# Performance work log

Hardware: AMD Instinct MI355X
Metric: run time of the kernel (lower is better)

## Reference

```python
import jax, jax.numpy as jnp
import numpy as np

B = 2_097_152  # batch of (ttm, logm) option quotes
J = 5          # hidden width from hidden_sizes=[5,5,5]


def setup_inputs() -> dict:
    key = jax.random.key(0)
    ks = jax.random.split(key, 14)
    d = jnp.float32
    s = 0.01  # torch init: normal(mean=0, std=0.01)
    inp = {
        "ttm": jax.random.uniform(ks[0], (B, 1), d),
        "logm": jax.random.normal(ks[1], (B, 1), d),
        "weights_logm": jax.random.normal(ks[2], (1, J), d) * s,
        "bias_logm": jax.random.normal(ks[3], (1, J), d) * s,
        "weights_ttm": jax.random.normal(ks[4], (1, J), d) * s,
        "bias_ttm": jax.random.normal(ks[5], (1, J), d) * s,
        "weights_exp": jax.random.normal(ks[6], (J, 1), d) * s,
        "bias_exp": jax.random.normal(ks[7], (1, J), d) * s,
        # nn.Linear default init ~ U(-1/sqrt(J), 1/sqrt(J))
        "W1": jax.random.uniform(ks[8], (J, J), d, -1.0, 1.0) / np.sqrt(J),
        "b1": jax.random.uniform(ks[9], (J,), d, -1.0, 1.0) / np.sqrt(J),
        "W2": jax.random.uniform(ks[10], (J, J), d, -1.0, 1.0) / np.sqrt(J),
        "b2": jax.random.uniform(ks[11], (J,), d, -1.0, 1.0) / np.sqrt(J),
        "Wo": jax.random.uniform(ks[12], (1, J), d, -1.0, 1.0) / np.sqrt(J),
        "bo": jax.random.uniform(ks[13], (1,), d, -1.0, 1.0) / np.sqrt(J),
    }
    return inp


def _forward(ttm, logm, weights_logm, bias_logm, weights_ttm, bias_ttm,
             weights_exp, bias_exp, W1, b1, W2, b2, Wo, bo):
    # smile transform of log-moneyness: sqrt(x*tanh(x+0.5) + tanh(-x/2) + 5e-4)
    x = bias_logm + logm @ jnp.exp(weights_logm)                     # [B, J]
    term_logm = jnp.sqrt(x * jnp.tanh(x + 0.5) + jnp.tanh(-x / 2) + 0.0005)
    term_ttm = jax.nn.sigmoid(bias_ttm + ttm @ jnp.exp(weights_ttm))  # [B, J]
    h = (term_logm * term_ttm) @ jnp.exp(weights_exp) + bias_exp      # [B,1]+[1,J] -> [B, J]
    h = jax.nn.softplus(h @ W1.T + b1)
    h = jax.nn.softplus(h @ W2.T + b2)
    return h @ Wo.T + bo                                              # [B, 1]


def reference(ttm, logm, weights_logm, bias_logm, weights_ttm, bias_ttm,
              weights_exp, bias_exp, W1, b1, W2, b2, Wo, bo):
    params = (weights_logm, bias_logm, weights_ttm, bias_ttm,
              weights_exp, bias_exp, W1, b1, W2, b2, Wo, bo)

    def out_sum(t, l):
        return jnp.sum(_forward(t, l, *params))

    output = _forward(ttm, logm, *params)                 # [B, 1]
    # grad of sum(output) wrt ttm and logm (rows independent -> per-sample grads)
    grad_ttm1, grad_logm1 = jax.grad(out_sum, argnums=(0, 1))(ttm, logm)
    # second derivative wrt logm: grad of sum(grad_logm1)
    grad_logm2 = jax.grad(
        lambda l: jnp.sum(jax.grad(out_sum, argnums=1)(ttm, l))
    )(logm)
    return (output, grad_ttm1, grad_logm1, grad_logm2)
```

## Files before the change

kernel.cpp:

```cpp
#include <hip/hip_runtime.h>
#include <math.h>

#define J 5

#if defined(__HIP_DEVICE_COMPILE__) && __has_builtin(__builtin_amdgcn_rcpf)
__device__ __forceinline__ float fastrcp(float x) { return __builtin_amdgcn_rcpf(x); }
#else
__device__ __forceinline__ float fastrcp(float x) { return 1.0f / x; }
#endif

#if defined(__HIP_DEVICE_COMPILE__) && __has_builtin(__builtin_amdgcn_rsqf)
__device__ __forceinline__ float fastrsq(float x) { return __builtin_amdgcn_rsqf(x); }
#else
__device__ __forceinline__ float fastrsq(float x) { return 1.0f / sqrtf(x); }
#endif

__device__ __forceinline__ float fast_tanh_from_e2y(float e2y) {
    return fmaf(-2.0f, fastrcp(e2y + 1.0f), 1.0f);
}

__global__ __launch_bounds__(256) void smile_kernel(
    const float* __restrict__ ttm,     const float* __restrict__ logm,
    const float* __restrict__ w_logm,  const float* __restrict__ b_logm,
    const float* __restrict__ w_ttm,   const float* __restrict__ b_ttm,
    const float* __restrict__ w_exp,   const float* __restrict__ b_exp,
    const float* __restrict__ W1,      const float* __restrict__ b1,
    const float* __restrict__ W2,      const float* __restrict__ b2,
    const float* __restrict__ Wo,      const float* __restrict__ bo,
    float* __restrict__ out, int n)
{
    const int tid = blockIdx.x * blockDim.x + threadIdx.x;
    const int i0  = tid * 4;
    if (i0 >= n) return;

    float ewl[J], bl[J], ewt[J], bt[J], ewe[J], wte[J];
#pragma unroll
    for (int j = 0; j < J; ++j) {
        ewl[j] = __expf(w_logm[j]);
        bl[j]  = b_logm[j];
        ewt[j] = __expf(w_ttm[j]);
        bt[j]  = b_ttm[j];
        ewe[j] = __expf(w_exp[j]);
        wte[j] = ewt[j] * ewe[j];
    }
    float r1[J], c1[J];
#pragma unroll
    for (int i = 0; i < J; ++i) {
        float r = 0.0f, c = b1[i];
#pragma unroll
        for (int j = 0; j < J; ++j) {
            const float w = W1[i * J + j];
            r += w;
            c = fmaf(w, b_exp[j], c);
        }
        r1[i] = r; c1[i] = c;
    }
    const float bo0 = bo[0];

    const float4 T4 = ((const float4*)ttm)[tid];
    const float4 L4 = ((const float4*)logm)[tid];
    float Ts[4] = {T4.x, T4.y, T4.z, T4.w};
    float Ls[4] = {L4.x, L4.y, L4.z, L4.w};
    float O0[4], O1[4], O2[4], O3[4];

#pragma unroll
    for (int k = 0; k < 4; ++k) {
        const float L = Ls[k], T = Ts[k];

        float s = 0.0f, sL = 0.0f, sLL = 0.0f, sT = 0.0f;
#pragma unroll
        for (int j = 0; j < J; ++j) {
            const float x  = fmaf(L, ewl[j], bl[j]);
            const float t1 = fast_tanh_from_e2y(__expf(fmaf(2.0f, x, 1.0f)));
            const float t2 = fast_tanh_from_e2y(__expf(-x));
            const float m1 = fmaf(-t1, t1, 1.0f);
            const float m2 = fmaf(-t2, t2, 1.0f);
            const float u  = fmaf(x, t1, t2) + 5.0e-4f;
            const float xm1 = x * m1;
            const float ux  = fmaf(-0.5f, m2, t1 + xm1);
            const float uxx = fmaf(-0.5f * t2, m2, 2.0f * fmaf(-t1, xm1, m1));
            const float r   = fastrsq(u);
            const float tl  = u * r;
            const float i2  = 0.5f * r;
            const float ru  = r * r;
            const float tlL  = ux * ewl[j] * i2;
            const float tlLL = (ewl[j] * ewl[j]) * i2 * fmaf(-0.5f * ux, ux * ru, uxx);
            const float z   = fmaf(T, ewt[j], bt[j]);
            const float tt  = fastrcp(1.0f + __expf(-z));
            const float dtt = fmaf(-tt, tt, tt);
            const float A   = tt * ewe[j];
            s   = fmaf(tl,   A, s);
            sL  = fmaf(tlL,  A, sL);
            sLL = fmaf(tlLL, A, sLL);
            sT  = fmaf(tl * dtt, wte[j], sT);
        }

        float h1[J], h1L[J], h1LL[J], h1T[J];
#pragma unroll
        for (int i = 0; i < J; ++i) {
            const float a   = fmaf(s, r1[i], c1[i]);
            const float aL  = sL  * r1[i];
            const float aLL = sLL * r1[i];
            const float aT  = sT  * r1[i];
            const float sg  = fastrcp(1.0f + __expf(-a));
            const float sp  = a - __logf(sg);
            const float dsg = fmaf(-sg, sg, sg);
            h1[i]   = sp;
            h1L[i]  = sg * aL;
            h1LL[i] = fmaf(dsg * aL, aL, sg * aLL);
            h1T[i]  = sg * aT;
        }

        float o = bo0, oL = 0.0f, oLL = 0.0f, oT = 0.0f;
#pragma unroll
        for (int i = 0; i < J; ++i) {
            float g = b2[i], gL = 0.0f, gLL = 0.0f, gT = 0.0f;
#pragma unroll
            for (int j = 0; j < J; ++j) {
                const float w = W2[i * J + j];
                g   = fmaf(w, h1[j],   g);
                gL  = fmaf(w, h1L[j],  gL);
                gLL = fmaf(w, h1LL[j], gLL);
                gT  = fmaf(w, h1T[j],  gT);
            }
            const float sg  = fastrcp(1.0f + __expf(-g));
            const float sp  = g - __logf(sg);
            const float dsg = fmaf(-sg, sg, sg);
            const float wo  = Wo[i];
            o   = fmaf(wo, sp, o);
            oL  = fmaf(wo, sg * gL, oL);
            oLL = fmaf(wo, fmaf(dsg * gL, gL, sg * gLL), oLL);
            oT  = fmaf(wo, sg * gT, oT);
        }

        O0[k] = o;
        O1[k] = oT;
        O2[k] = oL;
        O3[k] = oLL;
    }

    ((float4*)(out))[tid]                       = make_float4(O0[0], O0[1], O0[2], O0[3]);
    ((float4*)(out + (size_t)n))[tid]           = make_float4(O1[0], O1[1], O1[2], O1[3]);
    ((float4*)(out + 2 * (size_t)n))[tid]       = make_float4(O2[0], O2[1], O2[2], O2[3]);
    ((float4*)(out + 3 * (size_t)n))[tid]       = make_float4(O3[0], O3[1], O3[2], O3[3]);
}

extern "C" void kernel_launch(void* const* d_in, const int* in_sizes, int n_in,
                              void* d_out, int out_size, void* d_ws, size_t ws_size,
                              hipStream_t stream) {
    const float* ttm    = (const float*)d_in[0];
    const float* logm   = (const float*)d_in[1];
    const float* w_logm = (const float*)d_in[2];
    const float* b_logm = (const float*)d_in[3];
    const float* w_ttm  = (const float*)d_in[4];
    const float* b_ttm  = (const float*)d_in[5];
    const float* w_exp  = (const float*)d_in[6];
    const float* b_exp  = (const float*)d_in[7];
    const float* W1     = (const float*)d_in[8];
    const float* b1     = (const float*)d_in[9];
    const float* W2     = (const float*)d_in[10];
    const float* b2     = (const float*)d_in[11];
    const float* Wo     = (const float*)d_in[12];
    const float* bo     = (const float*)d_in[13];
    float* out = (float*)d_out;

    const int n = in_sizes[0];
    const int threads = (n + 3) / 4;
    const int blocks  = (threads + 255) / 256;
    smile_kernel<<<blocks, 256, 0, stream>>>(
        ttm, logm, w_logm, b_logm, w_ttm, b_ttm, w_exp, b_exp,
        W1, b1, W2, b2, Wo, bo, out, n);
}
```

Before: 125.0 us.

## Precompute weight constants in setup kernel and factor derivative propagation algebraically

A tiny setup kernel now precomputes the exponentiated weights, folded layer-1 coefficients and squared terms into workspace, so the main kernel stops recomputing them in every thread. The derivative chain is restructured: because every layer-1 pre-activation depends on one scalar, first and second derivatives are factored into shared terms (q, p, Bq, Bp), which removes the separate L/LL/T accumulators. Both tanh terms are computed from a single exp of x, and softplus uses a numerically stable abs-based form. This trades an extra kernel launch and a clamp on x for fewer transcendentals and FMAs per sample.

```diff
diff --git a/kernel.cpp b/kernel.cpp
--- a/kernel.cpp
+++ b/kernel.cpp
@@ -15,134 +15,173 @@
 __device__ __forceinline__ float fastrsq(float x) { return 1.0f / sqrtf(x); }
 #endif
 
-__device__ __forceinline__ float fast_tanh_from_e2y(float e2y) {
-    return fmaf(-2.0f, fastrcp(e2y + 1.0f), 1.0f);
-}
-
-__global__ __launch_bounds__(256) void smile_kernel(
-    const float* __restrict__ ttm,     const float* __restrict__ logm,
-    const float* __restrict__ w_logm,  const float* __restrict__ b_logm,
-    const float* __restrict__ w_ttm,   const float* __restrict__ b_ttm,
-    const float* __restrict__ w_exp,   const float* __restrict__ b_exp,
-    const float* __restrict__ W1,      const float* __restrict__ b1,
-    const float* __restrict__ W2,      const float* __restrict__ b2,
-    const float* __restrict__ Wo,      const float* __restrict__ bo,
-    float* __restrict__ out, int n)
+__global__ void setup_kernel(const float* __restrict__ w_logm, const float* __restrict__ b_logm,
+                             const float* __restrict__ w_ttm,  const float* __restrict__ b_ttm,
+                             const float* __restrict__ w_exp,  const float* __restrict__ b_exp,
+                             const float* __restrict__ W1,     const float* __restrict__ b1,
+                             const float* __restrict__ W2,     const float* __restrict__ b2,
+                             const float* __restrict__ Wo,     const float* __restrict__ bo,
+                             float* __restrict__ c)
+{
+    const int j = threadIdx.x;
+    if (j >= J) return;
+    const float ewl = __expf(w_logm[j]);
+    const float ewt = __expf(w_ttm[j]);
+    const float ewe = __expf(w_exp[j]);
+    c[0  + j] = ewl;
+    c[5  + j] = b_logm[j];
+    c[10 + j] = ewl * ewl;
+    c[15 + j] = -ewt;
+    c[20 + j] = -b_ttm[j];
+    c[25 + j] = ewe;
+    c[30 + j] = ewt * ewe;
+    float r = 0.0f, cc = b1[j];
+#pragma unroll
+    for (int t = 0; t < J; ++t) {
+        const float w = W1[j * J + t];
+        r += w;
+        cc = fmaf(w, b_exp[t], cc);
+    }
+    c[35 + j] = r;
+    c[40 + j] = cc;
+    c[45 + j] = r * r;
+#pragma unroll
+    for (int t = 0; t < J; ++t) c[50 + j * J + t] = W2[j * J + t];
+    c[75 + j] = b2[j];
+    c[80 + j] = Wo[j];
+    if (j == 0) c[85] = bo[0];
+}
+
+__device__ __forceinline__ void softplus_sig(float a, float& sp, float& sg) {
+    const float aa = fabsf(a);
+    const float em = __expf(-aa);
+    const float w  = fastrcp(1.0f + em);
+    sp = fmaxf(a, 0.0f) + __logf(1.0f + em);
+    sg = (a >= 0.0f) ? w : 1.0f - w;
+}
+
+__global__ __launch_bounds__(256) void smile_main(
+    const float* __restrict__ ttm, const float* __restrict__ logm,
+    const float* __restrict__ c, float* __restrict__ out, int n)
 {
     const int tid = blockIdx.x * blockDim.x + threadIdx.x;
-    const int i0  = tid * 4;
-    if (i0 >= n) return;
-
-    float ewl[J], bl[J], ewt[J], bt[J], ewe[J], wte[J];
+    if (tid * 4 >= n) return;
+
+    float ewl[J], bl[J], ewl2[J], newt[J], nbt[J], ewe[J], wte[J];
 #pragma unroll
     for (int j = 0; j < J; ++j) {
-        ewl[j] = __expf(w_logm[j]);
-        bl[j]  = b_logm[j];
-        ewt[j] = __expf(w_ttm[j]);
-        bt[j]  = b_ttm[j];
-        ewe[j] = __expf(w_exp[j]);
-        wte[j] = ewt[j] * ewe[j];
-    }
-    float r1[J], c1[J];
-#pragma unroll
-    for (int i = 0; i < J; ++i) {
-        float r = 0.0f, c = b1[i];
-#pragma unroll
-        for (int j = 0; j < J; ++j) {
-            const float w = W1[i * J + j];
-            r += w;
-            c = fmaf(w, b_exp[j], c);
-        }
-        r1[i] = r; c1[i] = c;
-    }
-    const float bo0 = bo[0];
+        ewl[j]  = c[0  + j];
+        bl[j]   = c[5  + j];
+        ewl2[j] = c[10 + j];
+        newt[j] = c[15 + j];
+        nbt[j]  = c[20 + j];
+        ewe[j]  = c[25 + j];
+        wte[j]  = c[30 + j];
+    }
 
     const float4 T4 = ((const float4*)ttm)[tid];
     const float4 L4 = ((const float4*)logm)[tid];
-    float Ts[4] = {T4.x, T4.y, T4.z, T4.w};
-    float Ls[4] = {L4.x, L4.y, L4.z, L4.w};
-    float O0[4], O1[4], O2[4], O3[4];
-
+    const float Ts[4] = {T4.x, T4.y, T4.z, T4.w};
+    const float Ls[4] = {L4.x, L4.y, L4.z, L4.w};
+
+    float sA[4], sLA[4], sLLA[4], sTA[4];
 #pragma unroll
     for (int k = 0; k < 4; ++k) {
         const float L = Ls[k], T = Ts[k];
-
         float s = 0.0f, sL = 0.0f, sLL = 0.0f, sT = 0.0f;
 #pragma unroll
         for (int j = 0; j < J; ++j) {
-            const float x  = fmaf(L, ewl[j], bl[j]);
-            const float t1 = fast_tanh_from_e2y(__expf(fmaf(2.0f, x, 1.0f)));
-            const float t2 = fast_tanh_from_e2y(__expf(-x));
+            float x = fmaf(L, ewl[j], bl[j]);
+            x = fminf(fmaxf(x, -30.0f), 30.0f);
+            const float ex = __expf(x);
+            const float e2 = ex * ex;
+            const float t1 = fmaf(-2.0f, fastrcp(fmaf(2.7182818284590452f, e2, 1.0f)), 1.0f);
+            const float t2 = (1.0f - ex) * fastrcp(1.0f + ex);
             const float m1 = fmaf(-t1, t1, 1.0f);
             const float m2 = fmaf(-t2, t2, 1.0f);
-            const float u  = fmaf(x, t1, t2) + 5.0e-4f;
+            const float u  = fmaf(x, t1, t2 + 5.0e-4f);
             const float xm1 = x * m1;
             const float ux  = fmaf(-0.5f, m2, t1 + xm1);
             const float uxx = fmaf(-0.5f * t2, m2, 2.0f * fmaf(-t1, xm1, m1));
             const float r   = fastrsq(u);
             const float tl  = u * r;
             const float i2  = 0.5f * r;
-            const float ru  = r * r;
-            const float tlL  = ux * ewl[j] * i2;
-            const float tlLL = (ewl[j] * ewl[j]) * i2 * fmaf(-0.5f * ux, ux * ru, uxx);
-            const float z   = fmaf(T, ewt[j], bt[j]);
-            const float tt  = fastrcp(1.0f + __expf(-z));
+            const float h   = ux * (r * r);
+            const float zn  = fmaf(T, newt[j], nbt[j]);
+            const float tt  = fastrcp(1.0f + __expf(zn));
             const float dtt = fmaf(-tt, tt, tt);
-            const float A   = tt * ewe[j];
-            s   = fmaf(tl,   A, s);
-            sL  = fmaf(tlL,  A, sL);
-            sLL = fmaf(tlLL, A, sLL);
+            const float AA   = tt * ewe[j];
+            const float ewlA = ewl[j] * AA;
+            s   = fmaf(tl, AA, s);
+            sL  = fmaf(ux * i2, ewlA, sL);
+            const float inner = fmaf(-0.5f * ux, h, uxx);
+            sLL = fmaf(inner * i2, ewl[j] * ewlA, sLL);
             sT  = fmaf(tl * dtt, wte[j], sT);
+            (void)ewl2;
         }
-
-        float h1[J], h1L[J], h1LL[J], h1T[J];
+        sA[k] = s; sLA[k] = sL; sLLA[k] = sLL; sTA[k] = sT;
+    }
+
+    float r1[J], c1[J], r1sq[J], W2r[J * J], b2[J], wo[J];
+#pragma unroll
+    for (int j = 0; j < J; ++j) {
+        r1[j]   = c[35 + j];
+        c1[j]   = c[40 + j];
+        r1sq[j] = c[45 + j];
+        b2[j]   = c[75 + j];
+        wo[j]   = c[80 + j];
+    }
+#pragma unroll
+    for (int t = 0; t < J * J; ++t) W2r[t] = c[50 + t];
+    const float bo0 = c[85];
+
+    float O0[4], O1[4], O2[4], O3[4];
+#pragma unroll
+    for (int k = 0; k < 4; ++k) {
+        const float s = sA[k], sL = sLA[k], sLL = sLLA[k], sT = sTA[k];
+
+        float q[J], p[J], sp1[J];
 #pragma unroll
         for (int i = 0; i < J; ++i) {
-            const float a   = fmaf(s, r1[i], c1[i]);
-            const float aL  = sL  * r1[i];
-            const float aLL = sLL * r1[i];
-            const float aT  = sT  * r1[i];
-            const float sg  = fastrcp(1.0f + __expf(-a));
-            const float sp  = a - __logf(sg);
+            const float a = fmaf(s, r1[i], c1[i]);
+            float sp, sg;
+            softplus_sig(a, sp, sg);
+            sp1[i] = sp;
+            q[i]   = sg * r1[i];
             const float dsg = fmaf(-sg, sg, sg);
-            h1[i]   = sp;
-            h1L[i]  = sg * aL;
-            h1LL[i] = fmaf(dsg * aL, aL, sg * aLL);
-            h1T[i]  = sg * aT;
+            p[i]   = dsg * r1sq[i];
         }
 
-        float o = bo0, oL = 0.0f, oLL = 0.0f, oT = 0.0f;
+        float o = bo0, u1 = 0.0f, u2 = 0.0f, u3 = 0.0f;
 #pragma unroll
         for (int i = 0; i < J; ++i) {
-            float g = b2[i], gL = 0.0f, gLL = 0.0f, gT = 0.0f;
+            float g = b2[i], Bq = 0.0f, Bp = 0.0f;
 #pragma unroll
             for (int j = 0; j < J; ++j) {
-                const float w = W2[i * J + j];
-                g   = fmaf(w, h1[j],   g);
-                gL  = fmaf(w, h1L[j],  gL);
-                gLL = fmaf(w, h1LL[j], gLL);
-                gT  = fmaf(w, h1T[j],  gT);
+                const float w = W2r[i * J + j];
+                g  = fmaf(w, sp1[j], g);
+                Bq = fmaf(w, q[j],   Bq);
+                Bp = fmaf(w, p[j],   Bp);
             }
-            const float sg  = fastrcp(1.0f + __expf(-g));
-            const float sp  = g - __logf(sg);
+            float sp, sg;
+            softplus_sig(g, sp, sg);
             const float dsg = fmaf(-sg, sg, sg);
-            const float wo  = Wo[i];
-            o   = fmaf(wo, sp, o);
-            oL  = fmaf(wo, sg * gL, oL);
-            oLL = fmaf(wo, fmaf(dsg * gL, gL, sg * gLL), oLL);
-            oT  = fmaf(wo, sg * gT, oT);
+            const float t   = wo[i] * sg;
+            o  = fmaf(wo[i], sp, o);
+            u1 = fmaf(t, Bq, u1);
+            u2 = fmaf(t, Bp, u2);
+            u3 = fmaf(wo[i] * dsg, Bq * Bq, u3);
         }
-
         O0[k] = o;
-        O1[k] = oT;
-        O2[k] = oL;
-        O3[k] = oLL;
-    }
-
-    ((float4*)(out))[tid]                       = make_float4(O0[0], O0[1], O0[2], O0[3]);
-    ((float4*)(out + (size_t)n))[tid]           = make_float4(O1[0], O1[1], O1[2], O1[3]);
-    ((float4*)(out + 2 * (size_t)n))[tid]       = make_float4(O2[0], O2[1], O2[2], O2[3]);
-    ((float4*)(out + 3 * (size_t)n))[tid]       = make_float4(O3[0], O3[1], O3[2], O3[3]);
+        O1[k] = sT * u1;
+        O2[k] = sL * u1;
+        O3[k] = fmaf(sL * sL, u3 + u2, sLL * u1);
+    }
+
+    ((float4*)(out))[tid]                 = make_float4(O0[0], O0[1], O0[2], O0[3]);
+    ((float4*)(out + (size_t)n))[tid]     = make_float4(O1[0], O1[1], O1[2], O1[3]);
+    ((float4*)(out + 2 * (size_t)n))[tid] = make_float4(O2[0], O2[1], O2[2], O2[3]);
+    ((float4*)(out + 3 * (size_t)n))[tid] = make_float4(O3[0], O3[1], O3[2], O3[3]);
 }
 
 extern "C" void kernel_launch(void* const* d_in, const int* in_sizes, int n_in,
@@ -163,11 +202,12 @@
     const float* Wo     = (const float*)d_in[12];
     const float* bo     = (const float*)d_in[13];
     float* out = (float*)d_out;
+    float* cns = (float*)d_ws;
 
     const int n = in_sizes[0];
+    setup_kernel<<<1, 64, 0, stream>>>(w_logm, b_logm, w_ttm, b_ttm, w_exp, b_exp,
+                                       W1, b1, W2, b2, Wo, bo, cns);
     const int threads = (n + 3) / 4;
     const int blocks  = (threads + 255) / 256;
-    smile_kernel<<<blocks, 256, 0, stream>>>(
-        ttm, logm, w_logm, b_logm, w_ttm, b_ttm, w_exp, b_exp,
-        W1, b1, W2, b2, Wo, bo, out, n);
-}
+    smile_main<<<blocks, 256, 0, stream>>>(ttm, logm, cns, out, n);
+}
```

Result: slower. 135.0 us (+8.0%).
